# Kernel tuning notes

Hardware: AMD Instinct MI355X
Metric: run time of the kernel (lower is better)

Reference implementation:

```python
import jax, jax.numpy as jnp
import numpy as np

DIM = 2048
N_HEADS = 32
N_KV_HEADS = 8
HEAD_DIM = DIM // N_HEADS  # 64
N_REP = N_HEADS // N_KV_HEADS  # 4
BSZ = 2
SEQ = 2048


def setup_inputs() -> dict:
    key = jax.random.key(0)
    ks = jax.random.split(key, 7)
    s = 0.02
    return {
        "x": jax.random.normal(ks[0], (BSZ, SEQ, DIM), dtype=jnp.float32),
        "freqs_cos": jnp.cos(jnp.outer(jnp.arange(SEQ, dtype=jnp.float32),
                                       1.0 / (10000.0 ** (jnp.arange(0, HEAD_DIM, 2, dtype=jnp.float32) / HEAD_DIM)))),
        "freqs_sin": jnp.sin(jnp.outer(jnp.arange(SEQ, dtype=jnp.float32),
                                       1.0 / (10000.0 ** (jnp.arange(0, HEAD_DIM, 2, dtype=jnp.float32) / HEAD_DIM)))),
        "wq": jax.random.normal(ks[1], (DIM, N_HEADS * HEAD_DIM), dtype=jnp.float32) * s,
        "wk": jax.random.normal(ks[2], (DIM, N_KV_HEADS * HEAD_DIM), dtype=jnp.float32) * s,
        "wv": jax.random.normal(ks[3], (DIM, N_KV_HEADS * HEAD_DIM), dtype=jnp.float32) * s,
        "wo": jax.random.normal(ks[4], (N_HEADS * HEAD_DIM, DIM), dtype=jnp.float32) * s,
    }


def _apply_rope(t, cos, sin):
    # t: [b, s, h, hd]; cos/sin: [s, hd/2] -> broadcast [1, s, 1, hd/2]
    tr = t.reshape(t.shape[:-1] + (HEAD_DIM // 2, 2))
    t_r, t_i = tr[..., 0], tr[..., 1]
    c = cos[None, :, None, :]
    s = sin[None, :, None, :]
    out_r = t_r * c - t_i * s
    out_i = t_r * s + t_i * c
    return jnp.stack([out_r, out_i], axis=-1).reshape(t.shape)


def reference(x, freqs_cos, freqs_sin, wq, wk, wv, wo):
    b, s, _ = x.shape
    xq = (x @ wq).reshape(b, s, N_HEADS, HEAD_DIM)
    xk = (x @ wk).reshape(b, s, N_KV_HEADS, HEAD_DIM)
    xv = (x @ wv).reshape(b, s, N_KV_HEADS, HEAD_DIM)

    xq = _apply_rope(xq, freqs_cos, freqs_sin)
    xk = _apply_rope(xk, freqs_cos, freqs_sin)

    # GQA: group query heads over kv heads instead of materializing repeated KV
    # xq -> [b, kv_heads, n_rep, s, hd]
    q = xq.transpose(0, 2, 1, 3).reshape(b, N_KV_HEADS, N_REP, s, HEAD_DIM)
    k = xk.transpose(0, 2, 1, 3)  # [b, kv, s, hd]
    v = xv.transpose(0, 2, 1, 3)  # [b, kv, s, hd]

    scale = 1.0 / jnp.sqrt(jnp.asarray(HEAD_DIM, dtype=x.dtype))
    scores = jnp.einsum("bgrqd,bgkd->bgrqk", q, k) * scale  # [b,kv,rep,s,s]
    causal = jnp.tril(jnp.ones((s, s), dtype=bool))
    scores = jnp.where(causal[None, None, None], scores, jnp.finfo(scores.dtype).min)
    probs = jax.nn.softmax(scores, axis=-1)
    out = jnp.einsum("bgrqk,bgkd->bgrqd", probs, v)  # [b,kv,rep,s,hd]
    out = out.reshape(b, N_HEADS, s, HEAD_DIM).transpose(0, 2, 1, 3).reshape(b, s, N_HEADS * HEAD_DIM)
    return out @ wo
```

## Files before the change

kernel.cpp:

```cpp
#include <hip/hip_runtime.h>

typedef unsigned short u16;
typedef unsigned int u32;
typedef __bf16 bf16x4 __attribute__((ext_vector_type(4)));
typedef __bf16 bf16x8 __attribute__((ext_vector_type(8)));
typedef float f32x4 __attribute__((ext_vector_type(4)));
typedef u32 u32x4 __attribute__((ext_vector_type(4)));

struct __align__(4) U16x2 { u16 x, y; };
struct __align__(8) U16x4 { u16 x, y, z, w; };

#define DEV static __device__ __forceinline__

extern "C" __device__ float __ocml_exp2_f32(float);
#if __has_builtin(__builtin_amdgcn_exp2f)
#define EXP2(x) __builtin_amdgcn_exp2f(x)
#else
#define EXP2(x) __ocml_exp2_f32(x)
#endif

DEV u16 f2bf(float f) {
  __bf16 h = (__bf16)f;
  return __builtin_bit_cast(u16, h);
}
DEV float bf2f(u16 u) { return __uint_as_float(((u32)u) << 16); }
DEV u32 pk2bf(float lo, float hi) { return (u32)f2bf(lo) | ((u32)f2bf(hi) << 16); }

DEV void gload16(const void* g, void* l) {
  __builtin_amdgcn_global_load_lds((const __attribute__((address_space(1))) char*)g,
                                   (__attribute__((address_space(3))) char*)l, 16, 0, 0);
}

DEV f32x4 mfma16(bf16x8 a, bf16x8 b, f32x4 c) {
  return __builtin_amdgcn_mfma_f32_16x16x32_bf16(a, b, c, 0, 0, 0);
}

__global__ __launch_bounds__(256) void cvt_x(const float* __restrict__ x, u16* __restrict__ xb) {
  int i = blockIdx.x * 256 + threadIdx.x;
  float4 v = ((const float4*)x)[i];
  U16x4 o;
  o.x = f2bf(v.x); o.y = f2bf(v.y); o.z = f2bf(v.z); o.w = f2bf(v.w);
  ((U16x4*)xb)[i] = o;
}

__global__ __launch_bounds__(256) void tconv(const float* __restrict__ src, u16* __restrict__ dst,
                                             int C, int nOff, int ldd) {
  __shared__ float t[32][33];
  int bx = blockIdx.x, by = blockIdx.y;
  int tx = threadIdx.x, ty = threadIdx.y;
#pragma unroll
  for (int j = 0; j < 4; ++j)
    t[ty + 8 * j][tx] = src[(size_t)(by * 32 + ty + 8 * j) * C + bx * 32 + tx];
  __syncthreads();
#pragma unroll
  for (int j = 0; j < 4; ++j)
    dst[(size_t)(nOff + bx * 32 + ty + 8 * j) * ldd + by * 32 + tx] = f2bf(t[tx][ty + 8 * j]);
}

__global__ __launch_bounds__(256) void vtrans(const u16* __restrict__ qkv, u16* __restrict__ Vt) {
  __shared__ u16 t[32][33];
  int bx = blockIdx.x, by = blockIdx.y, bz = blockIdx.z;
  int tx = threadIdx.x, ty = threadIdx.y;
  int b = bz >> 3, kh = bz & 7;
  const u16* src = qkv + (size_t)(b * 2048 + bx * 32) * 3072 + 2560 + kh * 64 + by * 32;
#pragma unroll
  for (int j = 0; j < 4; ++j) t[ty + 8 * j][tx] = src[(size_t)(ty + 8 * j) * 3072 + tx];
  __syncthreads();
  u16* dst = Vt + ((size_t)bz * 64 + by * 32) * 2048 + bx * 32;
#pragma unroll
  for (int j = 0; j < 4; ++j) dst[(size_t)(ty + 8 * j) * 2048 + tx] = t[tx][ty + 8 * j];
}

__global__ __launch_bounds__(256) void rope_qk(const u16* __restrict__ qkv,
                                               const float* __restrict__ fc,
                                               const float* __restrict__ fs,
                                               u16* __restrict__ Qo, u16* __restrict__ Ko) {
  int t = blockIdx.x * 256 + threadIdx.x;
  int d2 = t & 31;
  int rest = t >> 5;
  int h40 = rest % 40;
  int bs = rest / 40;
  int s = bs & 2047;
  int b = bs >> 11;
  const u16* src;
  u16* dst;
  float qscale;
  if (h40 < 32) {
    src = qkv + (size_t)bs * 3072 + h40 * 64 + 2 * d2;
    dst = Qo + (((size_t)(b * 32 + h40) * 2048 + s) * 64 + 2 * d2);
    qscale = 0.18033688011112042f;
  } else {
    int kh = h40 - 32;
    src = qkv + (size_t)bs * 3072 + 2048 + kh * 64 + 2 * d2;
    dst = Ko + (((size_t)(b * 8 + kh) * 2048 + s) * 64 + 2 * d2);
    qscale = 1.0f;
  }
  U16x2 v = *(const U16x2*)src;
  float xr = bf2f(v.x), xi = bf2f(v.y);
  float c = fc[s * 32 + d2] * qscale, sn = fs[s * 32 + d2] * qscale;
  U16x2 o;
  o.x = f2bf(xr * c - xi * sn);
  o.y = f2bf(xr * sn + xi * c);
  *(U16x2*)dst = o;
}

template <typename OutT>
__global__ __launch_bounds__(256, 2) void gemm_bt(const u16* __restrict__ A,
                                                  const u16* __restrict__ BT,
                                                  OutT* __restrict__ C,
                                                  int M, int N, int K) {
  __shared__ __align__(16) char smem[65536];
  const int tid = threadIdx.x;
  const int lane = tid & 63;
  const int wm = (tid >> 7) & 1, wn = (tid >> 6) & 1;
  const int tm = blockIdx.y, tn = blockIdx.x;
  const int Kb = K * 2;

  f32x4 acc[4][4];
#pragma unroll
  for (int i = 0; i < 4; ++i)
#pragma unroll
    for (int j = 0; j < 4; ++j) acc[i][j] = (f32x4){0.f, 0.f, 0.f, 0.f};

  const char* Ag = (const char*)A + (size_t)tm * 128 * Kb;
  const char* Bg = (const char*)BT + (size_t)tn * 128 * Kb;

  auto stage = [&](int buf, int t) {
#pragma unroll
    for (int i = 0; i < 4; ++i) {
      int vt = i * 256 + tid;
      int row = vt >> 3;
      int cb = (((vt & 7) << 4) ^ ((row & 7) << 4));
      gload16(Ag + (size_t)row * Kb + t * 128 + cb, smem + buf * 16384 + vt * 16);
      gload16(Bg + (size_t)row * Kb + t * 128 + cb, smem + 32768 + buf * 16384 + vt * 16);
    }
  };

  stage(0, 0);
  int cur = 0;
  const int NT = K >> 6;
  for (int t = 0; t < NT; ++t) {
    __syncthreads();
    if (t + 1 < NT) stage(cur ^ 1, t + 1);
    const char* As = smem + cur * 16384;
    const char* Bs = smem + 32768 + cur * 16384;
#pragma unroll
    for (int ks = 0; ks < 2; ++ks) {
      bf16x8 a[4], b[4];
#pragma unroll
      for (int mf = 0; mf < 4; ++mf) {
        int row = wm * 64 + mf * 16 + (lane & 15);
        int cb = (ks * 64 + ((lane >> 4) << 4)) ^ ((row & 7) << 4);
        a[mf] = *(const bf16x8*)(As + row * 128 + cb);
      }
#pragma unroll
      for (int nf = 0; nf < 4; ++nf) {
        int row = wn * 64 + nf * 16 + (lane & 15);
        int cb = (ks * 64 + ((lane >> 4) << 4)) ^ ((row & 7) << 4);
        b[nf] = *(const bf16x8*)(Bs + row * 128 + cb);
      }
#pragma unroll
      for (int mf = 0; mf < 4; ++mf)
#pragma unroll
        for (int nf = 0; nf < 4; ++nf) acc[mf][nf] = mfma16(a[mf], b[nf], acc[mf][nf]);
    }
    cur ^= 1;
  }
#pragma unroll
  for (int mf = 0; mf < 4; ++mf) {
    int row0 = tm * 128 + wm * 64 + mf * 16 + ((lane >> 4) << 2);
#pragma unroll
    for (int nf = 0; nf < 4; ++nf) {
      int col = tn * 128 + wn * 64 + nf * 16 + (lane & 15);
#pragma unroll
      for (int r = 0; r < 4; ++r) {
        float v = acc[mf][nf][r];
        if constexpr (sizeof(OutT) == 4)
          C[(size_t)(row0 + r) * N + col] = v;
        else
          C[(size_t)(row0 + r) * N + col] = f2bf(v);
      }
    }
  }
}

__global__ __launch_bounds__(128, 4) void attn(const u16* __restrict__ Q,
                                               const u16* __restrict__ Kt,
                                               const u16* __restrict__ Vt,
                                               u16* __restrict__ O) {
  __shared__ __align__(16) char smem[16384];

  const int tid = threadIdx.x, lane = tid & 63, w = tid >> 6;
  const int q15 = lane & 15, g = lane >> 4;
  const int bx = blockIdx.x, h = blockIdx.y, b = blockIdx.z;
  const int kh = h >> 2;
  const int QT0 = 63 - bx, QT1 = bx;

  const char* Qg = (const char*)(Q + ((size_t)(b * 32 + h) * 2048) * 64);
  const char* Kg = (const char*)(Kt + ((size_t)(b * 8 + kh) * 2048 * 64));
  const char* Vg = (const char*)(Vt + ((size_t)(b * 8 + kh) * 64 * 2048));

  bf16x8 qf0[2], qf1[2];
#pragma unroll
  for (int ks = 0; ks < 2; ++ks) {
    int r0 = QT0 * 32 + w * 16 + q15;
    int r1 = QT1 * 32 + w * 16 + q15;
    qf0[ks] = *(const bf16x8*)(Qg + (size_t)r0 * 128 + ks * 64 + (g << 4));
    qf1[ks] = *(const bf16x8*)(Qg + (size_t)r1 * 128 + ks * 64 + (g << 4));
  }

  f32x4 acc0[4], acc1[4];
#pragma unroll
  for (int j = 0; j < 4; ++j) {
    acc0[j] = (f32x4){0.f, 0.f, 0.f, 0.f};
    acc1[j] = (f32x4){0.f, 0.f, 0.f, 0.f};
  }
  float m0 = -1e30f, m1 = -1e30f, l0 = 0.f, l1 = 0.f;
  const f32x4 FZ = (f32x4){0.f, 0.f, 0.f, 0.f};

  auto stageKV = [&](int buf, int kt) {
#pragma unroll
    for (int i = 0; i < 2; ++i) {
      int vt = i * 128 + tid;
      int rho = vt >> 3, ck = vt & 7;
      int kap = ((rho & 12) << 1) + ((rho & 16) >> 2) + (rho & 3);
      gload16(Kg + (size_t)(kt * 32 + kap) * 128 + (((ck ^ rho) & 7) << 4),
              smem + buf * 8192 + vt * 16);
      int d = vt >> 2, cv = vt & 3;
      gload16(Vg + (size_t)d * 4096 + kt * 64 + (((cv ^ (d >> 1)) & 3) << 4),
              smem + buf * 8192 + 4096 + vt * 16);
    }
  };

  stageKV(0, 0);
  int cur = 0;
  const int nkt = QT0 + 1;
  for (int kt = 0; kt < nkt; ++kt) {
    __syncthreads();
    if (kt + 1 < nkt) stageKV(cur ^ 1, kt + 1);
    const char* Ks = smem + cur * 8192;
    const char* Vs = smem + cur * 8192 + 4096;
    const bool la = (kt <= QT1);

    bf16x8 kf[2][2];
#pragma unroll
    for (int ks = 0; ks < 2; ++ks)
#pragma unroll
      for (int nf = 0; nf < 2; ++nf) {
        int r = nf * 16 + q15;
        int c = (4 * ks + g) ^ (r & 7);
        kf[ks][nf] = *(const bf16x8*)(Ks + r * 128 + (c << 4));
      }

    f32x4 st0[2], st1[2];
    __builtin_amdgcn_s_setprio(1);
#pragma unroll
    for (int nf = 0; nf < 2; ++nf) {
      st0[nf] = mfma16(kf[0][nf], qf0[0], FZ);
      st0[nf] = mfma16(kf[1][nf], qf0[1], st0[nf]);
    }
    if (la) {
#pragma unroll
      for (int nf = 0; nf < 2; ++nf) {
        st1[nf] = mfma16(kf[0][nf], qf1[0], FZ);
        st1[nf] = mfma16(kf[1][nf], qf1[1], st1[nf]);
      }
    }
    __builtin_amdgcn_s_setprio(0);

    if (kt == QT0) {
      int qg = QT0 * 32 + w * 16 + q15;
#pragma unroll
      for (int nf = 0; nf < 2; ++nf)
#pragma unroll
        for (int r = 0; r < 4; ++r) {
          int kg = kt * 32 + 8 * g + 4 * nf + r;
          if (kg > qg) st0[nf][r] = -1e30f;
        }
    }
    if (la && kt == QT1) {
      int qg = QT1 * 32 + w * 16 + q15;
#pragma unroll
      for (int nf = 0; nf < 2; ++nf)
#pragma unroll
        for (int r = 0; r < 4; ++r) {
          int kg = kt * 32 + 8 * g + 4 * nf + r;
          if (kg > qg) st1[nf][r] = -1e30f;
        }
    }

    bf16x8 pa0, pa1;
#pragma unroll
    for (int t = 0; t < 2; ++t) {
      if (t == 1 && !la) break;
      f32x4* st = (t == 0) ? st0 : st1;
      float& m_r = (t == 0) ? m0 : m1;
      float& l_r = (t == 0) ? l0 : l1;
      f32x4* accT = (t == 0) ? acc0 : acc1;

      float vm = fmaxf(fmaxf(fmaxf(st[0][0], st[0][1]), fmaxf(st[0][2], st[0][3])),
                       fmaxf(fmaxf(st[1][0], st[1][1]), fmaxf(st[1][2], st[1][3])));
      vm = fmaxf(vm, __shfl_xor(vm, 16, 64));
      vm = fmaxf(vm, __shfl_xor(vm, 32, 64));
      const bool resc = !__all(vm - m_r <= 8.0f);
      if (resc) {
        float mn = fmaxf(m_r, vm);
        float cr = EXP2(m_r - mn);
        m_r = mn;
        l_r *= cr;
        float cra[4];
#pragma unroll
        for (int r = 0; r < 4; ++r) cra[r] = __shfl(cr, 4 * g + r, 64);
#pragma unroll
        for (int nfd = 0; nfd < 4; ++nfd)
#pragma unroll
          for (int r = 0; r < 4; ++r) accT[nfd][r] *= cra[r];
      }
      float vs = 0.f;
      u32x4 W;
      {
        float p0 = EXP2(st[0][0] - m_r), p1 = EXP2(st[0][1] - m_r);
        float p2 = EXP2(st[0][2] - m_r), p3 = EXP2(st[0][3] - m_r);
        float p4 = EXP2(st[1][0] - m_r), p5 = EXP2(st[1][1] - m_r);
        float p6 = EXP2(st[1][2] - m_r), p7 = EXP2(st[1][3] - m_r);
        vs = ((p0 + p1) + (p2 + p3)) + ((p4 + p5) + (p6 + p7));
        W.x = pk2bf(p0, p1);
        W.y = pk2bf(p2, p3);
        W.z = pk2bf(p4, p5);
        W.w = pk2bf(p6, p7);
      }
      if (t == 0) pa0 = __builtin_bit_cast(bf16x8, W);
      else pa1 = __builtin_bit_cast(bf16x8, W);
      vs += __shfl_xor(vs, 16, 64);
      vs += __shfl_xor(vs, 32, 64);
      l_r += vs;
    }

#pragma unroll
    for (int nfd = 0; nfd < 4; ++nfd) {
      int d = nfd * 16 + q15;
      int c = (g ^ (d >> 1)) & 3;
      bf16x8 vb = *(const bf16x8*)(Vs + d * 64 + (c << 4));
      __builtin_amdgcn_s_setprio(1);
      acc0[nfd] = mfma16(pa0, vb, acc0[nfd]);
      if (la) acc1[nfd] = mfma16(pa1, vb, acc1[nfd]);
      __builtin_amdgcn_s_setprio(0);
    }
    cur ^= 1;
  }

#pragma unroll
  for (int t = 0; t < 2; ++t) {
    float l_r = (t == 0) ? l0 : l1;
    f32x4* accT = (t == 0) ? acc0 : acc1;
    int qt = (t == 0) ? QT0 : QT1;
    u16* Og = O + ((size_t)(b * 2048 + qt * 32 + w * 16) * 2048 + h * 64);
    float la4[4];
#pragma unroll
    for (int r = 0; r < 4; ++r) la4[r] = __shfl(l_r, 4 * g + r, 64);
#pragma unroll
    for (int r = 0; r < 4; ++r) {
      float li = 1.f / la4[r];
#pragma unroll
      for (int nfd = 0; nfd < 4; ++nfd)
        Og[(size_t)(4 * g + r) * 2048 + nfd * 16 + q15] = f2bf(accT[nfd][r] * li);
    }
  }
}

extern "C" void kernel_launch(void* const* d_in, const int* in_sizes, int n_in,
                              void* d_out, int out_size, void* d_ws, size_t ws_size,
                              hipStream_t stream) {
  const float* x = (const float*)d_in[0];
  const float* fc = (const float*)d_in[1];
  const float* fs = (const float*)d_in[2];
  const float* wq = (const float*)d_in[3];
  const float* wk = (const float*)d_in[4];
  const float* wv = (const float*)d_in[5];
  const float* wo = (const float*)d_in[6];
  float* out = (float*)d_out;
  char* ws = (char*)d_ws;

  u16* xb    = (u16*)(ws);
  u16* qkv   = (u16*)(ws + 16777216);
  u16* woT   = (u16*)(ws + 41943040);
  u16* wqkvT = (u16*)(ws + 50331648);
  u16* Kbuf  = (u16*)(ws + 50331648);
  u16* Vtb   = (u16*)(ws + 54525952);
  u16* Qbuf = xb;
  u16* Obuf = qkv;

  dim3 tb(32, 8);
  cvt_x<<<dim3(8192), dim3(256), 0, stream>>>(x, xb);
  tconv<<<dim3(64, 64), tb, 0, stream>>>(wq, wqkvT, 2048, 0, 2048);
  tconv<<<dim3(16, 64), tb, 0, stream>>>(wk, wqkvT, 512, 2048, 2048);
  tconv<<<dim3(16, 64), tb, 0, stream>>>(wv, wqkvT, 512, 2560, 2048);
  tconv<<<dim3(64, 64), tb, 0, stream>>>(wo, woT, 2048, 0, 2048);
  gemm_bt<u16><<<dim3(24, 32), dim3(256), 0, stream>>>(xb, wqkvT, qkv, 4096, 3072, 2048);
  rope_qk<<<dim3(20480), dim3(256), 0, stream>>>(qkv, fc, fs, Qbuf, Kbuf);
  vtrans<<<dim3(64, 2, 16), tb, 0, stream>>>(qkv, Vtb);
  attn<<<dim3(32, 32, 2), dim3(128), 0, stream>>>(Qbuf, Kbuf, Vtb, Obuf);
  gemm_bt<float><<<dim3(16, 32), dim3(256), 0, stream>>>(Obuf, woT, out, 4096, 2048, 2048);
}
```

Before: 219.5 us.

## Fuse RoPE and Q/K/V scatter into QKV GEMM epilogue; defer softmax reductions

The QKV projection GEMM now applies rotary embedding and the Q scale in its epilogue, using a lane shuffle to fetch the paired element. It writes Q and K directly in head-major layout and V into a compact slice, which removes the separate rope kernel and its full round trip through global memory. In the attention loop, the cross-lane max reduction now runs only when a rescale is needed, and the row-sum reduction is moved out of the loop to the final normalisation. The trade-off is scattered 2-byte epilogue stores and extra frequency-table loads inside the GEMM.

```diff
diff --git a/kernel.cpp b/kernel.cpp
--- a/kernel.cpp
+++ b/kernel.cpp
@@ -23,7 +23,6 @@
   __bf16 h = (__bf16)f;
   return __builtin_bit_cast(u16, h);
 }
-DEV float bf2f(u16 u) { return __uint_as_float(((u32)u) << 16); }
 DEV u32 pk2bf(float lo, float hi) { return (u32)f2bf(lo) | ((u32)f2bf(hi) << 16); }
 
 DEV void gload16(const void* g, void* l) {
@@ -57,64 +56,33 @@
     dst[(size_t)(nOff + bx * 32 + ty + 8 * j) * ldd + by * 32 + tx] = f2bf(t[tx][ty + 8 * j]);
 }
 
-__global__ __launch_bounds__(256) void vtrans(const u16* __restrict__ qkv, u16* __restrict__ Vt) {
+__global__ __launch_bounds__(256) void vtrans(const u16* __restrict__ Vsl, u16* __restrict__ Vt) {
   __shared__ u16 t[32][33];
   int bx = blockIdx.x, by = blockIdx.y, bz = blockIdx.z;
   int tx = threadIdx.x, ty = threadIdx.y;
   int b = bz >> 3, kh = bz & 7;
-  const u16* src = qkv + (size_t)(b * 2048 + bx * 32) * 3072 + 2560 + kh * 64 + by * 32;
-#pragma unroll
-  for (int j = 0; j < 4; ++j) t[ty + 8 * j][tx] = src[(size_t)(ty + 8 * j) * 3072 + tx];
+  const u16* src = Vsl + (size_t)(b * 2048 + bx * 32) * 512 + kh * 64 + by * 32;
+#pragma unroll
+  for (int j = 0; j < 4; ++j) t[ty + 8 * j][tx] = src[(size_t)(ty + 8 * j) * 512 + tx];
   __syncthreads();
   u16* dst = Vt + ((size_t)bz * 64 + by * 32) * 2048 + bx * 32;
 #pragma unroll
   for (int j = 0; j < 4; ++j) dst[(size_t)(ty + 8 * j) * 2048 + tx] = t[tx][ty + 8 * j];
 }
 
-__global__ __launch_bounds__(256) void rope_qk(const u16* __restrict__ qkv,
-                                               const float* __restrict__ fc,
-                                               const float* __restrict__ fs,
-                                               u16* __restrict__ Qo, u16* __restrict__ Ko) {
-  int t = blockIdx.x * 256 + threadIdx.x;
-  int d2 = t & 31;
-  int rest = t >> 5;
-  int h40 = rest % 40;
-  int bs = rest / 40;
-  int s = bs & 2047;
-  int b = bs >> 11;
-  const u16* src;
-  u16* dst;
-  float qscale;
-  if (h40 < 32) {
-    src = qkv + (size_t)bs * 3072 + h40 * 64 + 2 * d2;
-    dst = Qo + (((size_t)(b * 32 + h40) * 2048 + s) * 64 + 2 * d2);
-    qscale = 0.18033688011112042f;
-  } else {
-    int kh = h40 - 32;
-    src = qkv + (size_t)bs * 3072 + 2048 + kh * 64 + 2 * d2;
-    dst = Ko + (((size_t)(b * 8 + kh) * 2048 + s) * 64 + 2 * d2);
-    qscale = 1.0f;
-  }
-  U16x2 v = *(const U16x2*)src;
-  float xr = bf2f(v.x), xi = bf2f(v.y);
-  float c = fc[s * 32 + d2] * qscale, sn = fs[s * 32 + d2] * qscale;
-  U16x2 o;
-  o.x = f2bf(xr * c - xi * sn);
-  o.y = f2bf(xr * sn + xi * c);
-  *(U16x2*)dst = o;
-}
-
-template <typename OutT>
-__global__ __launch_bounds__(256, 2) void gemm_bt(const u16* __restrict__ A,
-                                                  const u16* __restrict__ BT,
-                                                  OutT* __restrict__ C,
-                                                  int M, int N, int K) {
+__global__ __launch_bounds__(256, 2) void gemm_qkv(const u16* __restrict__ A,
+                                                   const u16* __restrict__ BT,
+                                                   const float* __restrict__ fc,
+                                                   const float* __restrict__ fs,
+                                                   u16* __restrict__ Qo,
+                                                   u16* __restrict__ Ko,
+                                                   u16* __restrict__ Vsl) {
   __shared__ __align__(16) char smem[65536];
   const int tid = threadIdx.x;
   const int lane = tid & 63;
   const int wm = (tid >> 7) & 1, wn = (tid >> 6) & 1;
   const int tm = blockIdx.y, tn = blockIdx.x;
-  const int Kb = K * 2;
+  const int K = 2048, Kb = 4096;
 
   f32x4 acc[4][4];
 #pragma unroll
@@ -166,20 +134,112 @@
     }
     cur ^= 1;
   }
+
+  const float QS = 0.18033688011112042f;
 #pragma unroll
   for (int mf = 0; mf < 4; ++mf) {
     int row0 = tm * 128 + wm * 64 + mf * 16 + ((lane >> 4) << 2);
 #pragma unroll
     for (int nf = 0; nf < 4; ++nf) {
       int col = tn * 128 + wn * 64 + nf * 16 + (lane & 15);
-#pragma unroll
-      for (int r = 0; r < 4; ++r) {
-        float v = acc[mf][nf][r];
-        if constexpr (sizeof(OutT) == 4)
-          C[(size_t)(row0 + r) * N + col] = v;
-        else
-          C[(size_t)(row0 + r) * N + col] = f2bf(v);
-      }
+      if (col < 2560) {
+        int d = col & 63, d2 = d >> 1;
+        bool ev = !(col & 1);
+        bool isQ = (col < 2048);
+        int hh = isQ ? (col >> 6) : ((col - 2048) >> 6);
+#pragma unroll
+        for (int r = 0; r < 4; ++r) {
+          int row = row0 + r;
+          int bb = row >> 11, s = row & 2047;
+          float v = acc[mf][nf][r];
+          float p = __shfl_xor(v, 1, 64);
+          float c = fc[s * 32 + d2], sn = fs[s * 32 + d2];
+          if (isQ) { c *= QS; sn *= QS; }
+          float o = ev ? (v * c - p * sn) : (v * c + p * sn);
+          if (isQ)
+            Qo[((size_t)(bb * 32 + hh) * 2048 + s) * 64 + d] = f2bf(o);
+          else
+            Ko[((size_t)(bb * 8 + hh) * 2048 + s) * 64 + d] = f2bf(o);
+        }
+      } else {
+#pragma unroll
+        for (int r = 0; r < 4; ++r)
+          Vsl[(size_t)(row0 + r) * 512 + (col - 2560)] = f2bf(acc[mf][nf][r]);
+      }
+    }
+  }
+}
+
+__global__ __launch_bounds__(256, 2) void gemm_bt(const u16* __restrict__ A,
+                                                  const u16* __restrict__ BT,
+                                                  float* __restrict__ C,
+                                                  int M, int N, int K) {
+  __shared__ __align__(16) char smem[65536];
+  const int tid = threadIdx.x;
+  const int lane = tid & 63;
+  const int wm = (tid >> 7) & 1, wn = (tid >> 6) & 1;
+  const int tm = blockIdx.y, tn = blockIdx.x;
+  const int Kb = K * 2;
+
+  f32x4 acc[4][4];
+#pragma unroll
+  for (int i = 0; i < 4; ++i)
+#pragma unroll
+    for (int j = 0; j < 4; ++j) acc[i][j] = (f32x4){0.f, 0.f, 0.f, 0.f};
+
+  const char* Ag = (const char*)A + (size_t)tm * 128 * Kb;
+  const char* Bg = (const char*)BT + (size_t)tn * 128 * Kb;
+
+  auto stage = [&](int buf, int t) {
+#pragma unroll
+    for (int i = 0; i < 4; ++i) {
+      int vt = i * 256 + tid;
+      int row = vt >> 3;
+      int cb = (((vt & 7) << 4) ^ ((row & 7) << 4));
+      gload16(Ag + (size_t)row * Kb + t * 128 + cb, smem + buf * 16384 + vt * 16);
+      gload16(Bg + (size_t)row * Kb + t * 128 + cb, smem + 32768 + buf * 16384 + vt * 16);
+    }
+  };
+
+  stage(0, 0);
+  int cur = 0;
+  const int NT = K >> 6;
+  for (int t = 0; t < NT; ++t) {
+    __syncthreads();
+    if (t + 1 < NT) stage(cur ^ 1, t + 1);
+    const char* As = smem + cur * 16384;
+    const char* Bs = smem + 32768 + cur * 16384;
+#pragma unroll
+    for (int ks = 0; ks < 2; ++ks) {
+      bf16x8 a[4], b[4];
+#pragma unroll
+      for (int mf = 0; mf < 4; ++mf) {
+        int row = wm * 64 + mf * 16 + (lane & 15);
+        int cb = (ks * 64 + ((lane >> 4) << 4)) ^ ((row & 7) << 4);
+        a[mf] = *(const bf16x8*)(As + row * 128 + cb);
+      }
+#pragma unroll
+      for (int nf = 0; nf < 4; ++nf) {
+        int row = wn * 64 + nf * 16 + (lane & 15);
+        int cb = (ks * 64 + ((lane >> 4) << 4)) ^ ((row & 7) << 4);
+        b[nf] = *(const bf16x8*)(Bs + row * 128 + cb);
+      }
+#pragma unroll
+      for (int mf = 0; mf < 4; ++mf)
+#pragma unroll
+        for (int nf = 0; nf < 4; ++nf) acc[mf][nf] = mfma16(a[mf], b[nf], acc[mf][nf]);
+    }
+    cur ^= 1;
+  }
+#pragma unroll
+  for (int mf = 0; mf < 4; ++mf) {
+    int row0 = tm * 128 + wm * 64 + mf * 16 + ((lane >> 4) << 2);
+#pragma unroll
+    for (int nf = 0; nf < 4; ++nf) {
+      int col = tn * 128 + wn * 64 + nf * 16 + (lane & 15);
+#pragma unroll
+      for (int r = 0; r < 4; ++r)
+        C[(size_t)(row0 + r) * N + col] = acc[mf][nf][r];
     }
   }
 }
@@ -300,10 +360,9 @@
 
       float vm = fmaxf(fmaxf(fmaxf(st[0][0], st[0][1]), fmaxf(st[0][2], st[0][3])),
                        fmaxf(fmaxf(st[1][0], st[1][1]), fmaxf(st[1][2], st[1][3])));
-      vm = fmaxf(vm, __shfl_xor(vm, 16, 64));
-      vm = fmaxf(vm, __shfl_xor(vm, 32, 64));
-      const bool resc = !__all(vm - m_r <= 8.0f);
-      if (resc) {
+      if (!__all(vm - m_r <= 8.0f)) {
+        vm = fmaxf(vm, __shfl_xor(vm, 16, 64));
+        vm = fmaxf(vm, __shfl_xor(vm, 32, 64));
         float mn = fmaxf(m_r, vm);
         float cr = EXP2(m_r - mn);
         m_r = mn;
@@ -316,24 +375,18 @@
 #pragma unroll
           for (int r = 0; r < 4; ++r) accT[nfd][r] *= cra[r];
       }
-      float vs = 0.f;
+      float p0 = EXP2(st[0][0] - m_r), p1 = EXP2(st[0][1] - m_r);
+      float p2 = EXP2(st[0][2] - m_r), p3 = EXP2(st[0][3] - m_r);
+      float p4 = EXP2(st[1][0] - m_r), p5 = EXP2(st[1][1] - m_r);
+      float p6 = EXP2(st[1][2] - m_r), p7 = EXP2(st[1][3] - m_r);
+      l_r += ((p0 + p1) + (p2 + p3)) + ((p4 + p5) + (p6 + p7));
       u32x4 W;
-      {
-        float p0 = EXP2(st[0][0] - m_r), p1 = EXP2(st[0][1] - m_r);
-        float p2 = EXP2(st[0][2] - m_r), p3 = EXP2(st[0][3] - m_r);
-        float p4 = EXP2(st[1][0] - m_r), p5 = EXP2(st[1][1] - m_r);
-        float p6 = EXP2(st[1][2] - m_r), p7 = EXP2(st[1][3] - m_r);
-        vs = ((p0 + p1) + (p2 + p3)) + ((p4 + p5) + (p6 + p7));
-        W.x = pk2bf(p0, p1);
-        W.y = pk2bf(p2, p3);
-        W.z = pk2bf(p4, p5);
-        W.w = pk2bf(p6, p7);
-      }
+      W.x = pk2bf(p0, p1);
+      W.y = pk2bf(p2, p3);
+      W.z = pk2bf(p4, p5);
+      W.w = pk2bf(p6, p7);
       if (t == 0) pa0 = __builtin_bit_cast(bf16x8, W);
       else pa1 = __builtin_bit_cast(bf16x8, W);
-      vs += __shfl_xor(vs, 16, 64);
-      vs += __shfl_xor(vs, 32, 64);
-      l_r += vs;
     }
 
 #pragma unroll
@@ -352,6 +405,8 @@
 #pragma unroll
   for (int t = 0; t < 2; ++t) {
     float l_r = (t == 0) ? l0 : l1;
+    l_r += __shfl_xor(l_r, 16, 64);
+    l_r += __shfl_xor(l_r, 32, 64);
     f32x4* accT = (t == 0) ? acc0 : acc1;
     int qt = (t == 0) ? QT0 : QT1;
     u16* Og = O + ((size_t)(b * 2048 + qt * 32 + w * 16) * 2048 + h * 64);
@@ -382,13 +437,13 @@
   char* ws = (char*)d_ws;
 
   u16* xb    = (u16*)(ws);
-  u16* qkv   = (u16*)(ws + 16777216);
-  u16* woT   = (u16*)(ws + 41943040);
-  u16* wqkvT = (u16*)(ws + 50331648);
-  u16* Kbuf  = (u16*)(ws + 50331648);
-  u16* Vtb   = (u16*)(ws + 54525952);
-  u16* Qbuf = xb;
-  u16* Obuf = qkv;
+  u16* Qb    = (u16*)(ws + 16777216);
+  u16* Kb    = (u16*)(ws + 33554432);
+  u16* Vsl   = (u16*)(ws + 37748736);
+  u16* Vtb   = (u16*)(ws + 41943040);
+  u16* woT   = (u16*)(ws + 46137344);
+  u16* wqkvT = (u16*)(ws + 54525952);
+  u16* Obuf = xb;
 
   dim3 tb(32, 8);
   cvt_x<<<dim3(8192), dim3(256), 0, stream>>>(x, xb);
@@ -396,9 +451,8 @@
   tconv<<<dim3(16, 64), tb, 0, stream>>>(wk, wqkvT, 512, 2048, 2048);
   tconv<<<dim3(16, 64), tb, 0, stream>>>(wv, wqkvT, 512, 2560, 2048);
   tconv<<<dim3(64, 64), tb, 0, stream>>>(wo, woT, 2048, 0, 2048);
-  gemm_bt<u16><<<dim3(24, 32), dim3(256), 0, stream>>>(xb, wqkvT, qkv, 4096, 3072, 2048);
-  rope_qk<<<dim3(20480), dim3(256), 0, stream>>>(qkv, fc, fs, Qbuf, Kbuf);
-  vtrans<<<dim3(64, 2, 16), tb, 0, stream>>>(qkv, Vtb);
-  attn<<<dim3(32, 32, 2), dim3(128), 0, stream>>>(Qbuf, Kbuf, Vtb, Obuf);
-  gemm_bt<float><<<dim3(16, 32), dim3(256), 0, stream>>>(Obuf, woT, out, 4096, 2048, 2048);
-}
+  gemm_qkv<<<dim3(24, 32), dim3(256), 0, stream>>>(xb, wqkvT, fc, fs, Qb, Kb, Vsl);
+  vtrans<<<dim3(64, 2, 16), tb, 0, stream>>>(Vsl, Vtb);
+  attn<<<dim3(32, 32, 2), dim3(128), 0, stream>>>(Qb, Kb, Vtb, Obuf);
+  gemm_bt<<<dim3(16, 32), dim3(256), 0, stream>>>(Obuf, woT, out, 4096, 2048, 2048);
+}
```

Result: faster. 203.8 us (-7.1%).
